# Kernel optimization log

Hardware: AMD Instinct MI355X
Metric: run time of the kernel (lower is better)

## Reference

```python
import jax, jax.numpy as jnp
import numpy as np

KH, KW = 3, 3
STRIDE, PAD, DIL = 1, 1, 1


def setup_inputs() -> dict:
    key = jax.random.key(0)
    k1, k2, k3, k4 = jax.random.split(key, 4)
    B, C, H, W = 4, 256, 64, 64
    O = 256
    x = jax.random.normal(k1, (B, C, H, W), dtype=jnp.float32)
    offset = jax.random.normal(k2, (B, 2 * KH * KW, H, W), dtype=jnp.float32)
    mask = jax.random.uniform(k3, (B, KH * KW, H, W), dtype=jnp.float32)
    weight = jax.random.normal(k4, (O, C, KH, KW), dtype=jnp.float32) * 0.02
    bias = jnp.zeros((O,), dtype=jnp.float32)
    return {"x": x, "offset": offset, "mask": mask, "weight": weight, "bias": bias}


def _bilinear_sample(x, py, px):
    # x: [B,C,H,W]; py,px: [B,K,Ho,Wo] fractional sample coords (zero outside)
    B, C, H, W = x.shape
    y0 = jnp.floor(py)
    x0 = jnp.floor(px)
    ly, lx = py - y0, px - x0
    hy, hx = 1.0 - ly, 1.0 - lx
    y0i = y0.astype(jnp.int32)
    x0i = x0.astype(jnp.int32)
    xf = x.reshape(B, C, H * W)

    def gather(yi, xi):
        valid = (yi >= 0) & (yi < H) & (xi >= 0) & (xi < W)
        yc = jnp.clip(yi, 0, H - 1)
        xc = jnp.clip(xi, 0, W - 1)
        idx = yc * W + xc  # [B,K,Ho,Wo]
        g = jax.vmap(lambda xb, ib: xb[:, ib.reshape(-1)])(xf, idx)  # [B,C,K*Ho*Wo]
        g = g.reshape(B, C, *yi.shape[1:])
        return g * valid[:, None].astype(x.dtype)

    return (gather(y0i, x0i) * (hy * hx)[:, None]
            + gather(y0i, x0i + 1) * (hy * lx)[:, None]
            + gather(y0i + 1, x0i) * (ly * hx)[:, None]
            + gather(y0i + 1, x0i + 1) * (ly * lx)[:, None])


def reference(x, offset, mask, weight, bias):
    B, C, H, W = x.shape
    O = weight.shape[0]
    K = KH * KW
    Ho = (H + 2 * PAD - DIL * (KH - 1) - 1) // STRIDE + 1
    Wo = (W + 2 * PAD - DIL * (KW - 1) - 1) // STRIDE + 1
    off = offset.reshape(B, K, 2, Ho, Wo)
    tap_y = (jnp.repeat(jnp.arange(KH), KW) * DIL).astype(x.dtype)  # [K]
    tap_x = (jnp.tile(jnp.arange(KW), KH) * DIL).astype(x.dtype)
    base_y = (jnp.arange(Ho) * STRIDE - PAD).astype(x.dtype)  # [Ho]
    base_x = (jnp.arange(Wo) * STRIDE - PAD).astype(x.dtype)
    py = off[:, :, 0] + base_y[None, None, :, None] + tap_y[None, :, None, None]
    px = off[:, :, 1] + base_x[None, None, None, :] + tap_x[None, :, None, None]
    # sampled columns: [B,C,K,Ho,Wo], modulated by mask
    val = _bilinear_sample(x, py, px) * mask[:, None]
    out = jnp.einsum('bckhw,ock->bohw', val, weight.reshape(O, C, K))
    return out + bias[None, :, None, None]
```

## Files before the change

### kernel.cpp

```cpp
#include <hip/hip_runtime.h>

typedef _Float16 f16x8 __attribute__((ext_vector_type(8)));
typedef float f32x4 __attribute__((ext_vector_type(4)));

__device__ __forceinline__ unsigned short f2h(float f) {
  union { _Float16 h; unsigned short u; } v;
  v.h = (_Float16)f;
  return v.u;
}
__device__ __forceinline__ f16x8 splat8(float w) {
  _Float16 h = (_Float16)w;
  f16x8 v = {h, h, h, h, h, h, h, h};
  return v;
}

__global__ __launch_bounds__(256) void prep_wx(
    const float* __restrict__ x, const float* __restrict__ w,
    unsigned short* __restrict__ xt, uint4* __restrict__ wfrag) {
  const int bid = blockIdx.x;
  const int t = threadIdx.x;
  if (bid >= 1024) {
    const int idx = (bid - 1024) * 256 + t;
    const int l = idx & 63;
    const int kt = (idx >> 6) % 72;
    const int g = idx / (72 * 64);
    const int o = g * 16 + (l & 15);
    const int kbase = kt * 32 + ((l >> 4) * 8);
    unsigned short h[8];
#pragma unroll
    for (int e = 0; e < 8; ++e) {
      const int klin = kbase + e;
      const int kk = klin >> 8;
      const int c = klin & 255;
      h[e] = f2h(w[((size_t)o * 256 + c) * 9 + kk]);
    }
    uint4 p;
    p.x = (unsigned)h[0] | ((unsigned)h[1] << 16);
    p.y = (unsigned)h[2] | ((unsigned)h[3] << 16);
    p.z = (unsigned)h[4] | ((unsigned)h[5] << 16);
    p.w = (unsigned)h[6] | ((unsigned)h[7] << 16);
    wfrag[idx] = p;
    return;
  }
  const int b = bid >> 8;
  const int h = (bid >> 2) & 63;
  const int cq = bid & 3;
  const int wave = t >> 6, lane = t & 63;
  __shared__ float lds[64][65];
  const int wpos = t >> 2, sub = t & 3;
  const int cl0 = wave * 4 + (lane >> 4);
  const int w0 = (lane & 15) * 4;
#pragma unroll
  for (int iter = 0; iter < 4; ++iter) {
    const int cl = iter * 16 + cl0;
    const int c = cq * 64 + cl;
    float4 v = *(const float4*)(x + (((size_t)b * 256 + c) * 64 + h) * 64 + w0);
    lds[cl][w0] = v.x; lds[cl][w0 + 1] = v.y;
    lds[cl][w0 + 2] = v.z; lds[cl][w0 + 3] = v.w;
  }
  __syncthreads();
  unsigned short hb[16];
#pragma unroll
  for (int j = 0; j < 16; ++j) hb[j] = f2h(lds[sub * 16 + j][wpos]);
  uint4 p0, p1;
  p0.x = (unsigned)hb[0] | ((unsigned)hb[1] << 16);
  p0.y = (unsigned)hb[2] | ((unsigned)hb[3] << 16);
  p0.z = (unsigned)hb[4] | ((unsigned)hb[5] << 16);
  p0.w = (unsigned)hb[6] | ((unsigned)hb[7] << 16);
  p1.x = (unsigned)hb[8] | ((unsigned)hb[9] << 16);
  p1.y = (unsigned)hb[10] | ((unsigned)hb[11] << 16);
  p1.z = (unsigned)hb[12] | ((unsigned)hb[13] << 16);
  p1.w = (unsigned)hb[14] | ((unsigned)hb[15] << 16);
  unsigned short* dst = xt + (((size_t)b * 64 + h) * 64 + wpos) * 256 + cq * 64 + sub * 16;
  *(uint4*)dst = p0;
  *(uint4*)(dst + 8) = p1;
}

__device__ __forceinline__ void combine8(uint4 q0, uint4 q1, uint4 q2, uint4 q3,
                                         float4 wt, _Float16* dst) {
  f16x8 t0, t1, t2, t3;
  __builtin_memcpy(&t0, &q0, 16);
  __builtin_memcpy(&t1, &q1, 16);
  __builtin_memcpy(&t2, &q2, 16);
  __builtin_memcpy(&t3, &q3, 16);
  f16x8 r = t0 * splat8(wt.x);
  r += t1 * splat8(wt.y);
  r += t2 * splat8(wt.z);
  r += t3 * splat8(wt.w);
  __builtin_memcpy(dst, &r, 16);
}

__global__ __launch_bounds__(512, 4) void dcn_fused(
    const unsigned short* __restrict__ xt, const float* __restrict__ off,
    const float* __restrict__ mask, const uint4* __restrict__ wfrag,
    const float* __restrict__ bias, float* __restrict__ out) {
  __shared__ __align__(16) _Float16 Bs[2][4096];
  __shared__ __align__(16) float swt[9 * 64 * 4];
  __shared__ __align__(16) int sidx[9 * 64 * 4];

  const int bid = blockIdx.x;
  const int id = ((bid & 7) << 6) | (bid >> 3);
  const int b = id >> 7;
  const int nt = (id >> 1) & 63;
  const int mh = id & 1;

  const int tid = threadIdx.x;
  const int lane = tid & 63;
  const int wv = tid >> 6;
  const int mg = wv & 3;
  const int nh2 = wv >> 2;
  const int lh = lane & 15, lg = lane >> 4;

  for (int pair = tid; pair < 576; pair += 512) {
    const int k = pair >> 6;
    const int pl = pair & 63;
    float oy = off[(((size_t)b * 18 + 2 * k) * 64 + nt) * 64 + pl];
    float ox = off[(((size_t)b * 18 + 2 * k + 1) * 64 + nt) * 64 + pl];
    float m = mask[(((size_t)b * 9 + k) * 64 + nt) * 64 + pl];
    float py = oy + (float)(nt - 1 + k / 3);
    float px = ox + (float)(pl - 1 + k % 3);
    float y0f = floorf(py), x0f = floorf(px);
    float ly = py - y0f, lx = px - x0f;
    float hy = 1.f - ly, hx = 1.f - lx;
    int y0 = (int)y0f, x0 = (int)x0f;
    int y1 = y0 + 1, x1 = x0 + 1;
    bool vy0 = (y0 >= 0) && (y0 < 64);
    bool vy1 = (y1 >= 0) && (y1 < 64);
    bool vx0 = (x0 >= 0) && (x0 < 64);
    bool vx1 = (x1 >= 0) && (x1 < 64);
    int yc0 = min(max(y0, 0), 63), yc1 = min(max(y1, 0), 63);
    int xc0 = min(max(x0, 0), 63), xc1 = min(max(x1, 0), 63);
    int* sp = sidx + (k * 64 + pl) * 4;
    float* wp = swt + (k * 64 + pl) * 4;
    sp[0] = (yc0 * 64 + xc0) * 256;
    sp[1] = (yc0 * 64 + xc1) * 256;
    sp[2] = (yc1 * 64 + xc0) * 256;
    sp[3] = (yc1 * 64 + xc1) * 256;
    wp[0] = (vy0 && vx0) ? hy * hx * m : 0.f;
    wp[1] = (vy0 && vx1) ? hy * lx * m : 0.f;
    wp[2] = (vy1 && vx0) ? ly * hx * m : 0.f;
    wp[3] = (vy1 && vx1) ? ly * lx * m : 0.f;
  }

  const uint4* aBase = wfrag + (size_t)(mh * 8 + mg * 2) * 4608 + lane;

  const int pos = tid >> 3, ci = tid & 7;
  const unsigned short* xtb = xt + (size_t)b * 1048576 + ci * 8;
  const int bsw = (ci >> 2) * 2048 + pos * 32 + (((ci & 3) ^ ((pos >> 1) & 3)) * 8);

  const int csw = (lg ^ ((lh >> 1) & 3)) * 8;
  int boff[2];
#pragma unroll
  for (int fn = 0; fn < 2; ++fn) boff[fn] = (nh2 * 32 + fn * 16 + lh) * 32 + csw;

#define LOADA(P, AR)                                                               \
  do {                                                                             \
    _Pragma("unroll") for (int j = 0; j < 4; ++j)                                  \
        AR[j] = aBase[(size_t)((((j & 1) * 72) + 2 * (P) + (j >> 1)) * 64)];       \
  } while (0)

#define LOADTAPS(Q0, Q1, Q2, Q3, IX, CO)                                           \
  do {                                                                             \
    Q0 = *(const uint4*)(xtb + (IX).x + (CO));                                     \
    Q1 = *(const uint4*)(xtb + (IX).y + (CO));                                     \
    Q2 = *(const uint4*)(xtb + (IX).z + (CO));                                     \
    Q3 = *(const uint4*)(xtb + (IX).w + (CO));                                     \
  } while (0)

#define MFMA_PHASE(BUF, AR)                                                        \
  do {                                                                             \
    const _Float16* Bb = &Bs[BUF][0];                                              \
    f16x8 b0[2], b1[2];                                                            \
    _Pragma("unroll") for (int fn = 0; fn < 2; ++fn) {                             \
      b0[fn] = *(const f16x8*)(Bb + boff[fn]);                                     \
      b1[fn] = *(const f16x8*)(Bb + 2048 + boff[fn]);                              \
    }                                                                              \
    __builtin_amdgcn_s_setprio(1);                                                 \
    _Pragma("unroll") for (int fm = 0; fm < 2; ++fm)                               \
        _Pragma("unroll") for (int fn = 0; fn < 2; ++fn) {                         \
      acc[fm][fn] = __builtin_amdgcn_mfma_f32_16x16x32_f16(                        \
          *(const f16x8*)&AR[fm], b0[fn], acc[fm][fn], 0, 0, 0);                   \
      acc[fm][fn] = __builtin_amdgcn_mfma_f32_16x16x32_f16(                        \
          *(const f16x8*)&AR[2 + fm], b1[fn], acc[fm][fn], 0, 0, 0);               \
    }                                                                              \
    __builtin_amdgcn_s_setprio(0);                                                 \
  } while (0)

#define BAR()                                                                      \
  do {                                                                             \
    asm volatile("s_waitcnt lgkmcnt(0)" ::: "memory");                             \
    __builtin_amdgcn_sched_barrier(0);                                             \
    __builtin_amdgcn_s_barrier();                                                  \
    __builtin_amdgcn_sched_barrier(0);                                             \
  } while (0)

#define PHASE(P_, AL, AC, QL0, QL1, QL2, QL3, QC0, QC1, QC2, QC3)                  \
  do {                                                                             \
    LOADA((P_) + 1, AL);                                                           \
    int4 ix = *(const int4*)(sidx + ((((P_) + 2) >> 2) * 64 + pos) * 4);           \
    LOADTAPS(QL0, QL1, QL2, QL3, ix, (((P_) + 2) & 3) * 64);                       \
    float4 wt4 = *(const float4*)(swt + ((((P_) + 1) >> 2) * 64 + pos) * 4);       \
    MFMA_PHASE((P_) & 1, AC);                                                      \
    combine8(QC0, QC1, QC2, QC3, wt4, &Bs[((P_) + 1) & 1][0] + bsw);               \
    BAR();                                                                         \
  } while (0)

  f32x4 acc[2][2] = {};
  uint4 AE[4], AO[4];
  uint4 qA0, qA1, qA2, qA3, qB0, qB1, qB2, qB3;

  __syncthreads();

  {
    float4 wt0 = *(const float4*)(swt + pos * 4);
    int4 ix0 = *(const int4*)(sidx + pos * 4);
    LOADTAPS(qA0, qA1, qA2, qA3, ix0, 0);
    combine8(qA0, qA1, qA2, qA3, wt0, &Bs[0][0] + bsw);
    LOADA(0, AE);
    LOADTAPS(qB0, qB1, qB2, qB3, ix0, 64);
    BAR();
  }

  for (int p = 0; p < 34; p += 2) {
    PHASE(p, AO, AE, qA0, qA1, qA2, qA3, qB0, qB1, qB2, qB3);
    PHASE(p + 1, AE, AO, qB0, qB1, qB2, qB3, qA0, qA1, qA2, qA3);
  }
  {
    LOADA(35, AO);
    float4 wt4 = *(const float4*)(swt + (8 * 64 + pos) * 4);
    MFMA_PHASE(0, AE);
    combine8(qB0, qB1, qB2, qB3, wt4, &Bs[1][0] + bsw);
    BAR();
    MFMA_PHASE(1, AO);
  }

  float* outb = out + (size_t)b * 1048576 + (size_t)nt * 64 + nh2 * 32;
#pragma unroll
  for (int fm = 0; fm < 2; ++fm) {
#pragma unroll
    for (int i = 0; i < 4; ++i) {
      const int o = mh * 128 + mg * 32 + fm * 16 + lg * 4 + i;
      const float bs = bias[o];
      float* orow = outb + (size_t)o * 4096 + lh;
#pragma unroll
      for (int fn = 0; fn < 2; ++fn) orow[fn * 16] = acc[fm][fn][i] + bs;
    }
  }
#undef LOADA
#undef LOADTAPS
#undef MFMA_PHASE
#undef BAR
#undef PHASE
}

extern "C" void kernel_launch(void* const* d_in, const int* in_sizes, int n_in,
                              void* d_out, int out_size, void* d_ws, size_t ws_size,
                              hipStream_t stream) {
  const float* x = (const float*)d_in[0];
  const float* off = (const float*)d_in[1];
  const float* mask = (const float*)d_in[2];
  const float* wgt = (const float*)d_in[3];
  const float* bias = (const float*)d_in[4];
  float* out = (float*)d_out;

  uint4* wfrag = (uint4*)d_ws;
  unsigned short* xtp = (unsigned short*)(wfrag + 73728);

  prep_wx<<<1312, 256, 0, stream>>>(x, wgt, xtp, wfrag);
  dcn_fused<<<512, 512, 0, stream>>>(xtp, off, mask, wfrag, bias, out);
}
```

Measured before the change: 55.94 us.

## Make each wave build its own B tile to remove block barriers

The fused deformable-conv kernel is restructured so that each wave gathers and combines the bilinear samples for its own 32 positions into a private LDS slice, then runs MFMAs on it directly. This removes the per-phase block-wide barrier. Blocks shrink from 512 to 256 threads, and each wave now covers 64 output channels by 32 positions over 72 k-steps of 32 channels. The cost is more gathered loads per thread, more registers for the accumulators and prefetch buffers, and lower occupancy per block, with each wave handling twice the M dimension.

Result: slower. 98.13 us (+75.4%).

```diff
diff --git a/kernel.cpp b/kernel.cpp
--- a/kernel.cpp
+++ b/kernel.cpp
@@ -77,7 +77,7 @@
 }
 
 __device__ __forceinline__ void combine8(uint4 q0, uint4 q1, uint4 q2, uint4 q3,
-                                         float4 wt, _Float16* dst) {
+                                         float4 wt, uint4* dst) {
   f16x8 t0, t1, t2, t3;
   __builtin_memcpy(&t0, &q0, 16);
   __builtin_memcpy(&t1, &q1, 16);
@@ -90,11 +90,11 @@
   __builtin_memcpy(dst, &r, 16);
 }
 
-__global__ __launch_bounds__(512, 4) void dcn_fused(
+__global__ __launch_bounds__(256, 2) void dcn_fused(
     const unsigned short* __restrict__ xt, const float* __restrict__ off,
     const float* __restrict__ mask, const uint4* __restrict__ wfrag,
     const float* __restrict__ bias, float* __restrict__ out) {
-  __shared__ __align__(16) _Float16 Bs[2][4096];
+  __shared__ __align__(16) _Float16 Bw[4][2][1024];
   __shared__ __align__(16) float swt[9 * 64 * 4];
   __shared__ __align__(16) int sidx[9 * 64 * 4];
 
@@ -107,16 +107,16 @@
   const int tid = threadIdx.x;
   const int lane = tid & 63;
   const int wv = tid >> 6;
-  const int mg = wv & 3;
-  const int nh2 = wv >> 2;
+  const int mg = wv >> 1;
+  const int ph = wv & 1;
   const int lh = lane & 15, lg = lane >> 4;
 
-  for (int pair = tid; pair < 576; pair += 512) {
-    const int k = pair >> 6;
-    const int pl = pair & 63;
+  for (int e = tid; e < 576; e += 256) {
+    const int k = e >> 6;
+    const int pl = e & 63;
     float oy = off[(((size_t)b * 18 + 2 * k) * 64 + nt) * 64 + pl];
     float ox = off[(((size_t)b * 18 + 2 * k + 1) * 64 + nt) * 64 + pl];
-    float m = mask[(((size_t)b * 9 + k) * 64 + nt) * 64 + pl];
+    float mk = mask[(((size_t)b * 9 + k) * 64 + nt) * 64 + pl];
     float py = oy + (float)(nt - 1 + k / 3);
     float px = ox + (float)(pl - 1 + k % 3);
     float y0f = floorf(py), x0f = floorf(px);
@@ -130,127 +130,106 @@
     bool vx1 = (x1 >= 0) && (x1 < 64);
     int yc0 = min(max(y0, 0), 63), yc1 = min(max(y1, 0), 63);
     int xc0 = min(max(x0, 0), 63), xc1 = min(max(x1, 0), 63);
-    int* sp = sidx + (k * 64 + pl) * 4;
+    int* sp_ = sidx + (k * 64 + pl) * 4;
     float* wp = swt + (k * 64 + pl) * 4;
-    sp[0] = (yc0 * 64 + xc0) * 256;
-    sp[1] = (yc0 * 64 + xc1) * 256;
-    sp[2] = (yc1 * 64 + xc0) * 256;
-    sp[3] = (yc1 * 64 + xc1) * 256;
-    wp[0] = (vy0 && vx0) ? hy * hx * m : 0.f;
-    wp[1] = (vy0 && vx1) ? hy * lx * m : 0.f;
-    wp[2] = (vy1 && vx0) ? ly * hx * m : 0.f;
-    wp[3] = (vy1 && vx1) ? ly * lx * m : 0.f;
-  }
-
-  const uint4* aBase = wfrag + (size_t)(mh * 8 + mg * 2) * 4608 + lane;
-
-  const int pos = tid >> 3, ci = tid & 7;
-  const unsigned short* xtb = xt + (size_t)b * 1048576 + ci * 8;
-  const int bsw = (ci >> 2) * 2048 + pos * 32 + (((ci & 3) ^ ((pos >> 1) & 3)) * 8);
-
-  const int csw = (lg ^ ((lh >> 1) & 3)) * 8;
-  int boff[2];
-#pragma unroll
-  for (int fn = 0; fn < 2; ++fn) boff[fn] = (nh2 * 32 + fn * 16 + lh) * 32 + csw;
-
-#define LOADA(P, AR)                                                               \
+    sp_[0] = (yc0 * 64 + xc0) * 256;
+    sp_[1] = (yc0 * 64 + xc1) * 256;
+    sp_[2] = (yc1 * 64 + xc0) * 256;
+    sp_[3] = (yc1 * 64 + xc1) * 256;
+    wp[0] = (vy0 && vx0) ? hy * hx * mk : 0.f;
+    wp[1] = (vy0 && vx1) ? hy * lx * mk : 0.f;
+    wp[2] = (vy1 && vx0) ? ly * hx * mk : 0.f;
+    wp[3] = (vy1 && vx1) ? ly * lx * mk : 0.f;
+  }
+  __syncthreads();
+
+  const int sp = lane >> 1;
+  const int ch2 = lane & 1;
+  const int cg0 = ch2 * 2;
+  const int gpos = ph * 32 + sp;
+  const unsigned short* xtb = xt + (size_t)b * 1048576;
+
+  const uint4* aBase = wfrag + (size_t)(mh * 8 + mg * 4) * 4608 + lane;
+
+  _Float16* bw = &Bw[wv][0][0];
+  const int wr0 = sp * 32 + ((cg0 ^ ((sp >> 1) & 3)) * 8);
+  const int wr1 = sp * 32 + (((cg0 + 1) ^ ((sp >> 1) & 3)) * 8);
+  const int rd0 = (0 * 16 + lh) * 32 + ((lg ^ ((lh >> 1) & 3)) * 8);
+  const int rd1 = (1 * 16 + lh) * 32 + ((lg ^ ((lh >> 1) & 3)) * 8);
+
+#define LOADTAPS(T, Q)                                                             \
+  do {                                                                             \
+    int4 ix = *(const int4*)(sidx + (((T) >> 3) * 64 + gpos) * 4);                 \
+    const int co = ((T) & 7) * 32;                                                 \
+    Q[0] = *(const uint4*)(xtb + ix.x + co + cg0 * 8);                             \
+    Q[1] = *(const uint4*)(xtb + ix.y + co + cg0 * 8);                             \
+    Q[2] = *(const uint4*)(xtb + ix.z + co + cg0 * 8);                             \
+    Q[3] = *(const uint4*)(xtb + ix.w + co + cg0 * 8);                             \
+    Q[4] = *(const uint4*)(xtb + ix.x + co + cg0 * 8 + 8);                         \
+    Q[5] = *(const uint4*)(xtb + ix.y + co + cg0 * 8 + 8);                         \
+    Q[6] = *(const uint4*)(xtb + ix.z + co + cg0 * 8 + 8);                         \
+    Q[7] = *(const uint4*)(xtb + ix.w + co + cg0 * 8 + 8);                         \
+  } while (0)
+
+#define LOADA(T, AR)                                                               \
   do {                                                                             \
     _Pragma("unroll") for (int j = 0; j < 4; ++j)                                  \
-        AR[j] = aBase[(size_t)((((j & 1) * 72) + 2 * (P) + (j >> 1)) * 64)];       \
+        AR[j] = aBase[(size_t)(j * 4608 + (T) * 64)];                              \
   } while (0)
 
-#define LOADTAPS(Q0, Q1, Q2, Q3, IX, CO)                                           \
+#define ITER(T, QC, QL, AC, AL, DOLOAD)                                            \
   do {                                                                             \
-    Q0 = *(const uint4*)(xtb + (IX).x + (CO));                                     \
-    Q1 = *(const uint4*)(xtb + (IX).y + (CO));                                     \
-    Q2 = *(const uint4*)(xtb + (IX).z + (CO));                                     \
-    Q3 = *(const uint4*)(xtb + (IX).w + (CO));                                     \
-  } while (0)
-
-#define MFMA_PHASE(BUF, AR)                                                        \
-  do {                                                                             \
-    const _Float16* Bb = &Bs[BUF][0];                                              \
-    f16x8 b0[2], b1[2];                                                            \
-    _Pragma("unroll") for (int fn = 0; fn < 2; ++fn) {                             \
-      b0[fn] = *(const f16x8*)(Bb + boff[fn]);                                     \
-      b1[fn] = *(const f16x8*)(Bb + 2048 + boff[fn]);                              \
+    if (DOLOAD) {                                                                  \
+      LOADTAPS((T) + 1, QL);                                                       \
+      LOADA((T) + 1, AL);                                                          \
     }                                                                              \
+    float4 wt4 = *(const float4*)(swt + (((T) >> 3) * 64 + gpos) * 4);             \
+    uint4 r0, r1;                                                                  \
+    combine8(QC[0], QC[1], QC[2], QC[3], wt4, &r0);                                \
+    combine8(QC[4], QC[5], QC[6], QC[7], wt4, &r1);                                \
+    _Float16* bb = bw + ((T) & 1) * 1024;                                          \
+    *(uint4*)(bb + wr0) = r0;                                                      \
+    *(uint4*)(bb + wr1) = r1;                                                      \
+    f16x8 fr0 = *(const f16x8*)(bb + rd0);                                         \
+    f16x8 fr1 = *(const f16x8*)(bb + rd1);                                         \
     __builtin_amdgcn_s_setprio(1);                                                 \
-    _Pragma("unroll") for (int fm = 0; fm < 2; ++fm)                               \
-        _Pragma("unroll") for (int fn = 0; fn < 2; ++fn) {                         \
-      acc[fm][fn] = __builtin_amdgcn_mfma_f32_16x16x32_f16(                        \
-          *(const f16x8*)&AR[fm], b0[fn], acc[fm][fn], 0, 0, 0);                   \
-      acc[fm][fn] = __builtin_amdgcn_mfma_f32_16x16x32_f16(                        \
-          *(const f16x8*)&AR[2 + fm], b1[fn], acc[fm][fn], 0, 0, 0);               \
+    _Pragma("unroll") for (int j = 0; j < 4; ++j) {                                \
+      acc[j][0] = __builtin_amdgcn_mfma_f32_16x16x32_f16(                          \
+          *(const f16x8*)&AC[j], fr0, acc[j][0], 0, 0, 0);                         \
+      acc[j][1] = __builtin_amdgcn_mfma_f32_16x16x32_f16(                          \
+          *(const f16x8*)&AC[j], fr1, acc[j][1], 0, 0, 0);                         \
     }                                                                              \
     __builtin_amdgcn_s_setprio(0);                                                 \
   } while (0)
 
-#define BAR()                                                                      \
-  do {                                                                             \
-    asm volatile("s_waitcnt lgkmcnt(0)" ::: "memory");                             \
-    __builtin_amdgcn_sched_barrier(0);                                             \
-    __builtin_amdgcn_s_barrier();                                                  \
-    __builtin_amdgcn_sched_barrier(0);                                             \
-  } while (0)
-
-#define PHASE(P_, AL, AC, QL0, QL1, QL2, QL3, QC0, QC1, QC2, QC3)                  \
-  do {                                                                             \
-    LOADA((P_) + 1, AL);                                                           \
-    int4 ix = *(const int4*)(sidx + ((((P_) + 2) >> 2) * 64 + pos) * 4);           \
-    LOADTAPS(QL0, QL1, QL2, QL3, ix, (((P_) + 2) & 3) * 64);                       \
-    float4 wt4 = *(const float4*)(swt + ((((P_) + 1) >> 2) * 64 + pos) * 4);       \
-    MFMA_PHASE((P_) & 1, AC);                                                      \
-    combine8(QC0, QC1, QC2, QC3, wt4, &Bs[((P_) + 1) & 1][0] + bsw);               \
-    BAR();                                                                         \
-  } while (0)
-
-  f32x4 acc[2][2] = {};
-  uint4 AE[4], AO[4];
-  uint4 qA0, qA1, qA2, qA3, qB0, qB1, qB2, qB3;
-
-  __syncthreads();
-
-  {
-    float4 wt0 = *(const float4*)(swt + pos * 4);
-    int4 ix0 = *(const int4*)(sidx + pos * 4);
-    LOADTAPS(qA0, qA1, qA2, qA3, ix0, 0);
-    combine8(qA0, qA1, qA2, qA3, wt0, &Bs[0][0] + bsw);
-    LOADA(0, AE);
-    LOADTAPS(qB0, qB1, qB2, qB3, ix0, 64);
-    BAR();
-  }
-
-  for (int p = 0; p < 34; p += 2) {
-    PHASE(p, AO, AE, qA0, qA1, qA2, qA3, qB0, qB1, qB2, qB3);
-    PHASE(p + 1, AE, AO, qB0, qB1, qB2, qB3, qA0, qA1, qA2, qA3);
-  }
-  {
-    LOADA(35, AO);
-    float4 wt4 = *(const float4*)(swt + (8 * 64 + pos) * 4);
-    MFMA_PHASE(0, AE);
-    combine8(qB0, qB1, qB2, qB3, wt4, &Bs[1][0] + bsw);
-    BAR();
-    MFMA_PHASE(1, AO);
-  }
-
-  float* outb = out + (size_t)b * 1048576 + (size_t)nt * 64 + nh2 * 32;
-#pragma unroll
-  for (int fm = 0; fm < 2; ++fm) {
+  f32x4 acc[4][2] = {};
+  uint4 qE[8], qO[8], AE[4], AO[4];
+
+  LOADTAPS(0, qE);
+  LOADA(0, AE);
+
+  for (int p = 0; p < 69; p += 2) {
+    ITER(p, qE, qO, AE, AO, 1);
+    ITER(p + 1, qO, qE, AO, AE, 1);
+  }
+  ITER(70, qE, qO, AE, AO, 1);
+  ITER(71, qO, qE, AO, AE, 0);
+
+  float* outb = out + (size_t)b * 1048576 + (size_t)nt * 64 + ph * 32;
+#pragma unroll
+  for (int j = 0; j < 4; ++j) {
 #pragma unroll
     for (int i = 0; i < 4; ++i) {
-      const int o = mh * 128 + mg * 32 + fm * 16 + lg * 4 + i;
+      const int o = (mh * 8 + mg * 4 + j) * 16 + lg * 4 + i;
       const float bs = bias[o];
       float* orow = outb + (size_t)o * 4096 + lh;
 #pragma unroll
-      for (int fn = 0; fn < 2; ++fn) orow[fn * 16] = acc[fm][fn][i] + bs;
+      for (int fn = 0; fn < 2; ++fn) orow[fn * 16] = acc[j][fn][i] + bs;
     }
   }
+#undef LOADTAPS
 #undef LOADA
-#undef LOADTAPS
-#undef MFMA_PHASE
-#undef BAR
-#undef PHASE
+#undef ITER
 }
 
 extern "C" void kernel_launch(void* const* d_in, const int* in_sizes, int n_in,
@@ -267,5 +246,5 @@
   unsigned short* xtp = (unsigned short*)(wfrag + 73728);
 
   prep_wx<<<1312, 256, 0, stream>>>(x, wgt, xtp, wfrag);
-  dcn_fused<<<512, 512, 0, stream>>>(xtp, off, mask, wfrag, bias, out);
-}
+  dcn_fused<<<512, 256, 0, stream>>>(xtp, off, mask, wfrag, bias, out);
+}
```
